# Optimization experiments

Measured on AMD Instinct MI355X. Metric: run time of the kernel, lower is better.

Reference implementation:

```python
import jax, jax.numpy as jnp
import numpy as np

B, N, DIM = 8, 8192, 256
HEADS, LOCAL_HEADS, WINDOW = 8, 1, 64
HD = DIM // HEADS  # 32
MLP_HIDDEN = 1024
EPS = 1e-5


def layer_norm(x, g, b):
    mu = jnp.mean(x, axis=-1, keepdims=True)
    var = jnp.var(x, axis=-1, keepdims=True)
    return (x - mu) * jax.lax.rsqrt(var + EPS) * g + b


def look_around(t, pad_value=0.0):
    # t: (b, nw, w, ...); concat windows [i-1, i, i+1] -> (b, nw, 3w, ...)
    nw = t.shape[1]
    pads = [(0, 0), (1, 1)] + [(0, 0)] * (t.ndim - 2)
    p = jnp.pad(t, pads, constant_values=pad_value)
    return jnp.concatenate([p[:, i:i + nw] for i in range(3)], axis=2)


def local_attn(q, k, v):
    # lucidrains LocalAttention, causal=False, look_backward=look_forward=1
    # q,k,v: (b_merged, n, d)
    b, n, d = q.shape
    nw = n // WINDOW
    scale = d ** -0.5
    bq = q.reshape(b, nw, WINDOW, d) * scale
    bk = look_around(k.reshape(b, nw, WINDOW, d))  # (b, nw, 3w, d)
    bv = look_around(v.reshape(b, nw, WINDOW, d))
    ticker = jnp.arange(n).reshape(1, nw, WINDOW)
    bq_k = look_around(ticker, pad_value=-1)       # (1, nw, 3w)
    pad_mask = (bq_k == -1)[:, :, None, :]         # (1, nw, 1, 3w)
    dots = jnp.einsum('bnie,bnje->bnij', bq, bk)   # (b, nw, w, 3w)
    dots = jnp.where(pad_mask, -1e9, dots)
    attn = jax.nn.softmax(dots, axis=-1)
    out = jnp.einsum('bnij,bnje->bnie', attn, bv)
    return out.reshape(b, n, d)


def linear_attn(q, k, v):
    # q,k,v: (b, h, n, d)
    d = q.shape[-1]
    qs = jax.nn.softmax(q, axis=-1) * d ** -0.5
    ks = jax.nn.softmax(k, axis=-2)
    ctx = jnp.einsum('bhnd,bhne->bhde', ks, v)     # (b, h, d, d) tiny
    return jnp.einsum('bhnd,bhde->bhne', qs, ctx)


def setup_inputs() -> dict:
    key = jax.random.key(0)
    ks = jax.random.split(key, 8)
    s = 0.02
    return {
        'x': jax.random.normal(ks[0], (B, N, DIM), jnp.float32),
        'norm1_g': jnp.ones((DIM,), jnp.float32),
        'norm1_b': jnp.zeros((DIM,), jnp.float32),
        'Wq': jax.random.normal(ks[1], (DIM, DIM), jnp.float32) * s,
        'Wkv': jax.random.normal(ks[2], (DIM, DIM), jnp.float32) * s,
        'Wproj': jax.random.normal(ks[3], (DIM, DIM), jnp.float32) * s,
        'bproj': jnp.zeros((DIM,), jnp.float32),
        'norm2_g': jnp.ones((DIM,), jnp.float32),
        'norm2_b': jnp.zeros((DIM,), jnp.float32),
        'W1': jax.random.normal(ks[4], (MLP_HIDDEN, DIM), jnp.float32) * s,
        'b1': jnp.zeros((MLP_HIDDEN,), jnp.float32),
        'W2': jax.random.normal(ks[5], (DIM, MLP_HIDDEN), jnp.float32) * s,
        'b2': jnp.zeros((DIM,), jnp.float32),
    }


def reference(x, norm1_g, norm1_b, Wq, Wkv, Wproj, bproj, norm2_g, norm2_b, W1, b1, W2, b2):
    b, n, c = x.shape
    h = layer_norm(x, norm1_g, norm1_b)
    q = h @ Wq.T
    kv = h @ Wkv.T  # k and v share the same projection in the original code
    split_heads = lambda t: t.reshape(b, n, HEADS, HD).transpose(0, 2, 1, 3)
    q, k, v = split_heads(q), split_heads(kv), split_heads(kv)
    lq, gq = q[:, :LOCAL_HEADS], q[:, LOCAL_HEADS:]
    lk, gk = k[:, :LOCAL_HEADS], k[:, LOCAL_HEADS:]
    lv, gv = v[:, :LOCAL_HEADS], v[:, LOCAL_HEADS:]
    lout = local_attn(lq.reshape(b * LOCAL_HEADS, n, HD),
                      lk.reshape(b * LOCAL_HEADS, n, HD),
                      lv.reshape(b * LOCAL_HEADS, n, HD)).reshape(b, LOCAL_HEADS, n, HD)
    gout = linear_attn(gq, gk, gv)
    attn = jnp.concatenate([lout, gout], axis=1)   # (b, H, n, hd)
    y = attn.transpose(0, 2, 1, 3).reshape(b, n, c) @ Wproj.T + bproj
    x = x + y
    h2 = layer_norm(x, norm2_g, norm2_b)
    m = jax.nn.gelu(h2 @ W1.T + b1, approximate=False) @ W2.T + b2
    return x + m
```

## Files before the change

### kernel.cpp

```cpp
#include <hip/hip_runtime.h>
#include <hip/hip_bf16.h>

typedef __bf16 bf16;
typedef __bf16 bf16x8 __attribute__((ext_vector_type(8)));
typedef float f32x4 __attribute__((ext_vector_type(4)));

__device__ __forceinline__ void gld16(const void* g, void* l) {
  __builtin_amdgcn_global_load_lds((const __attribute__((address_space(1))) void*)g,
                                   (__attribute__((address_space(3))) void*)l, 16, 0, 0);
}

__global__ void cvt_weights(const float* __restrict__ wq, const float* __restrict__ wkv,
                            const float* __restrict__ wp, const float* __restrict__ w1,
                            const float* __restrict__ w2,
                            bf16* __restrict__ wqkv, bf16* __restrict__ wpb,
                            bf16* __restrict__ w1b, bf16* __restrict__ w2b) {
  int i = blockIdx.x * 256 + threadIdx.x;
  if (i < 65536) wqkv[i] = (bf16)wq[i];
  else if (i < 131072) wqkv[i] = (bf16)wkv[i - 65536];
  else if (i < 196608) wpb[i - 131072] = (bf16)wp[i - 131072];
  else if (i < 458752) w1b[i - 196608] = (bf16)w1[i - 196608];
  else if (i < 720896) w2b[i - 458752] = (bf16)w2[i - 458752];
}

__launch_bounds__(256)
__global__ void ln_kernel(const float* __restrict__ x, const float* __restrict__ g,
                          const float* __restrict__ b, bf16* __restrict__ out) {
  const int row = blockIdx.x * 4 + (threadIdx.x >> 6);
  const int lane = threadIdx.x & 63;
  const float4 v = ((const float4*)(x + (long)row * 256))[lane];
  float s = v.x + v.y + v.z + v.w;
#pragma unroll
  for (int o = 1; o < 64; o <<= 1) s += __shfl_xor(s, o);
  const float mu = s * (1.f / 256.f);
  const float dx = v.x - mu, dy = v.y - mu, dz = v.z - mu, dw = v.w - mu;
  float q = dx * dx + dy * dy + dz * dz + dw * dw;
#pragma unroll
  for (int o = 1; o < 64; o <<= 1) q += __shfl_xor(q, o);
  const float rstd = rsqrtf(q * (1.f / 256.f) + 1e-5f);
  const float4 gg = ((const float4*)g)[lane];
  const float4 bb = ((const float4*)b)[lane];
  union { bf16 h[4]; uint2 u; } pk;
  pk.h[0] = (bf16)(dx * rstd * gg.x + bb.x);
  pk.h[1] = (bf16)(dy * rstd * gg.y + bb.y);
  pk.h[2] = (bf16)(dz * rstd * gg.z + bb.z);
  pk.h[3] = (bf16)(dw * rstd * gg.w + bb.w);
  *(uint2*)(out + (long)row * 256 + lane * 4) = pk.u;
}

template <int EPI, int MT, int NTILE, int KK, int NCHUNK>
__launch_bounds__(512, 4)
__global__ void gemm_bd(const bf16* __restrict__ A, const bf16* __restrict__ B,
                        void* C, const float* __restrict__ bias,
                        const float* res, int ldC) {
  constexpr int CW = NTILE / 8;
  constexpr int FM = MT / 16;
  constexpr int FN = CW / 16;
  constexpr int CK = KK / NCHUNK;
  constexpr int RSB = 2 * CK;
  constexpr int LROW = (RSB == 256) ? 8 : ((RSB == 512) ? 9 : 10);
  constexpr int CHB = MT * CK * 2;
  constexpr int ITER = CHB / (512 * 16);
  __shared__ bf16 lds[2 * MT * CK];
  const int tid = threadIdx.x;
  const int w = tid >> 6, lane = tid & 63;
  const int l15 = lane & 15, l4 = lane >> 4;
  const int swz = (l15 & 7) << 4;
  const long m0 = (long)blockIdx.x * MT;
  const int n_base = blockIdx.y * NTILE;
  const bf16* Bl = B + ((long)(n_base + w * CW + l15)) * KK + l4 * 8;

  f32x4 acc[FM][FN] = {};

  auto stage = [&](int c, int buf) {
#pragma unroll
    for (int it = 0; it < ITER; ++it) {
      const int p = it * 8192 + tid * 16;
      const int row = p >> LROW;
      const int colb = (p & (RSB - 1)) ^ ((row & 7) << 4);
      gld16((const char*)A + ((m0 + row) * KK + (long)c * CK) * 2 + colb,
            (char*)lds + buf * CHB + it * 8192 + w * 1024);
    }
  };

  stage(0, 0);
  asm volatile("s_waitcnt vmcnt(0)" ::: "memory");
  __syncthreads();

  for (int c = 0; c < NCHUNK; ++c) {
    if (c + 1 < NCHUNK) stage(c + 1, (c + 1) & 1);
    const char* base = (const char*)lds + (c & 1) * CHB;
#pragma unroll
    for (int kl = 0; kl < CK / 32; ++kl) {
      bf16x8 bfrag[FN];
#pragma unroll
      for (int fn = 0; fn < FN; ++fn)
        bfrag[fn] = *(const bf16x8*)(Bl + (long)fn * 16 * KK + c * CK + kl * 32);
      bf16x8 afrag[FM];
#pragma unroll
      for (int fm = 0; fm < FM; ++fm)
        afrag[fm] = *(const bf16x8*)(base + (fm * 16 + l15) * RSB + ((kl * 64 + l4 * 16) ^ swz));
#pragma unroll
      for (int fm = 0; fm < FM; ++fm)
#pragma unroll
        for (int fn = 0; fn < FN; ++fn)
          acc[fm][fn] = __builtin_amdgcn_mfma_f32_16x16x32_bf16(afrag[fm], bfrag[fn], acc[fm][fn], 0, 0, 0);
    }
    if (c + 1 < NCHUNK) {
      asm volatile("s_waitcnt vmcnt(0)" ::: "memory");
      __syncthreads();
    }
  }

#pragma unroll
  for (int fm = 0; fm < FM; ++fm)
#pragma unroll
    for (int fn = 0; fn < FN; ++fn)
#pragma unroll
      for (int r = 0; r < 4; ++r) {
        const long row = m0 + fm * 16 + l4 * 4 + r;
        const int col = n_base + w * CW + fn * 16 + l15;
        const long idx = row * ldC + col;
        const float v = acc[fm][fn][r];
        if constexpr (EPI == 0) {
          ((bf16*)C)[idx] = (bf16)v;
        } else if constexpr (EPI == 1) {
          ((float*)C)[idx] = v + bias[col] + res[idx];
        } else {
          const float t = v + bias[col];
          ((bf16*)C)[idx] = (bf16)(0.5f * t * (1.f + erff(t * 0.70710678118654752f)));
        }
      }
}

__launch_bounds__(256)
__global__ void lattn_kernel(const bf16* __restrict__ qkv, bf16* __restrict__ attn) {
  const int j = blockIdx.x, b = blockIdx.y;
  const int tid = threadIdx.x, w = tid >> 6, lane = tid & 63;
  __shared__ bf16 Qs[64 * 40];
  __shared__ bf16 Ks[192 * 40];
  __shared__ bf16 Kt[32 * 200];
  __shared__ bf16 Ps[4][16 * 200];
  const float scale = 0.17677669529663687f;
  const long base = (long)b * 8192 + (long)j * 64;
  for (int i = tid; i < 64 * 32; i += 256) {
    const int r = i >> 5, d = i & 31;
    Qs[r * 40 + d] = (bf16)((float)qkv[(base + r) * 512 + d] * scale);
  }
  for (int i = tid; i < 192 * 32; i += 256) {
    const int c = i >> 5, d = i & 31;
    const long tc = (long)j * 64 - 64 + c;
    float kv = 0.f;
    if (tc >= 0 && tc < 8192) kv = (float)qkv[((long)b * 8192 + tc) * 512 + 256 + d];
    const bf16 kb = (bf16)kv;
    Ks[c * 40 + d] = kb;
    Kt[d * 200 + c] = kb;
  }
  __syncthreads();
  const int l15 = lane & 15, l4 = lane >> 4;
  const bf16x8 aq = *(const bf16x8*)(Qs + (w * 16 + l15) * 40 + l4 * 8);
  const f32x4 zz = {0.f, 0.f, 0.f, 0.f};
  f32x4 S[12];
#pragma unroll
  for (int fn = 0; fn < 12; ++fn) {
    const bf16x8 bk = *(const bf16x8*)(Ks + (fn * 16 + l15) * 40 + l4 * 8);
    S[fn] = __builtin_amdgcn_mfma_f32_16x16x32_bf16(aq, bk, zz, 0, 0, 0);
  }
#pragma unroll
  for (int fn = 0; fn < 12; ++fn) {
    const long tc = (long)j * 64 - 64 + fn * 16 + l15;
    if (tc < 0 || tc >= 8192) { S[fn][0] = -1e9f; S[fn][1] = -1e9f; S[fn][2] = -1e9f; S[fn][3] = -1e9f; }
  }
  float sinv[4];
#pragma unroll
  for (int r = 0; r < 4; ++r) {
    float m = -1e30f;
#pragma unroll
    for (int fn = 0; fn < 12; ++fn) m = fmaxf(m, S[fn][r]);
#pragma unroll
    for (int o = 1; o < 16; o <<= 1) m = fmaxf(m, __shfl_xor(m, o));
    float s = 0.f;
#pragma unroll
    for (int fn = 0; fn < 12; ++fn) { const float e = __expf(S[fn][r] - m); S[fn][r] = e; s += e; }
#pragma unroll
    for (int o = 1; o < 16; o <<= 1) s += __shfl_xor(s, o);
    sinv[r] = 1.f / s;
  }
#pragma unroll
  for (int fn = 0; fn < 12; ++fn)
#pragma unroll
    for (int r = 0; r < 4; ++r)
      Ps[w][(l4 * 4 + r) * 200 + fn * 16 + l15] = (bf16)(S[fn][r] * sinv[r]);
  __syncthreads();
  f32x4 O[2] = {};
#pragma unroll
  for (int ks = 0; ks < 6; ++ks) {
    const bf16x8 ap = *(const bf16x8*)(Ps[w] + l15 * 200 + ks * 32 + l4 * 8);
#pragma unroll
    for (int fe = 0; fe < 2; ++fe) {
      const bf16x8 bv = *(const bf16x8*)(Kt + (fe * 16 + l15) * 200 + ks * 32 + l4 * 8);
      O[fe] = __builtin_amdgcn_mfma_f32_16x16x32_bf16(ap, bv, O[fe], 0, 0, 0);
    }
  }
#pragma unroll
  for (int fe = 0; fe < 2; ++fe)
#pragma unroll
    for (int r = 0; r < 4; ++r)
      attn[(base + w * 16 + l4 * 4 + r) * 256 + fe * 16 + l15] = (bf16)O[fe][r];
}

__launch_bounds__(256)
__global__ void ctx_kernel(const bf16* __restrict__ qkv, float* __restrict__ ctx,
                           float* __restrict__ S) {
  const int bh = blockIdx.x;
  const int b = bh / 7, h = bh % 7 + 1;
  const int tid = threadIdx.x;
  const int w = tid >> 6, lane = tid & 63;
  const int l15 = lane & 15, l4 = lane >> 4;
  __shared__ bf16 evT[32 * 264];
  __shared__ bf16 kT[48 * 264];
  __shared__ float red[4][32 * 48];
  const long n0 = (long)blockIdx.y * 256;
  const bf16* kp = qkv + ((long)b * 8192 + n0 + tid) * 512 + 256 + h * 32;
  bf16x8 kv[4];
#pragma unroll
  for (int c = 0; c < 4; ++c) kv[c] = *(const bf16x8*)(kp + c * 8);
#pragma unroll
  for (int i = 0; i < 16; ++i)
    kT[(32 + i) * 264 + tid] = (i == 0) ? (bf16)1.0f : (bf16)0.0f;
#pragma unroll
  for (int c = 0; c < 4; ++c)
#pragma unroll
    for (int j = 0; j < 8; ++j) {
      const int d = c * 8 + j;
      evT[d * 264 + tid] = (bf16)__expf((float)kv[c][j]);
      kT[d * 264 + tid] = kv[c][j];
    }
  __syncthreads();
  f32x4 acc[2][3] = {};
#pragma unroll
  for (int ks = 0; ks < 2; ++ks) {
    const int ncol = w * 64 + ks * 32 + l4 * 8;
    bf16x8 af[2], bb[3];
#pragma unroll
    for (int fm = 0; fm < 2; ++fm) af[fm] = *(const bf16x8*)(evT + (fm * 16 + l15) * 264 + ncol);
#pragma unroll
    for (int fe = 0; fe < 3; ++fe) bb[fe] = *(const bf16x8*)(kT + (fe * 16 + l15) * 264 + ncol);
#pragma unroll
    for (int fm = 0; fm < 2; ++fm)
#pragma unroll
      for (int fe = 0; fe < 3; ++fe)
        acc[fm][fe] = __builtin_amdgcn_mfma_f32_16x16x32_bf16(af[fm], bb[fe], acc[fm][fe], 0, 0, 0);
  }
#pragma unroll
  for (int fm = 0; fm < 2; ++fm)
#pragma unroll
    for (int fe = 0; fe < 3; ++fe)
#pragma unroll
      for (int r = 0; r < 4; ++r)
        red[w][(fm * 16 + l4 * 4 + r) * 48 + fe * 16 + l15] = acc[fm][fe][r];
  __syncthreads();
  for (int i = tid; i < 32 * 48; i += 256) {
    const float v = red[0][i] + red[1][i] + red[2][i] + red[3][i];
    const int d = i / 48, e = i - d * 48;
    if (e < 32) atomicAdd(ctx + (long)bh * 1024 + d * 32 + e, v);
    else if (e == 32) atomicAdd(S + bh * 32 + d, v);
  }
}

__launch_bounds__(256)
__global__ void lout_kernel(const bf16* __restrict__ qkv, const float* __restrict__ S,
                            const float* __restrict__ ctx, bf16* __restrict__ attn) {
  const int bh = blockIdx.x;
  const int b = bh / 7, h = bh % 7 + 1;
  const int tid = threadIdx.x;
  const int w = tid >> 6, lane = tid & 63;
  const int l15 = lane & 15, l4 = lane >> 4;
  __shared__ bf16 qs[256 * 40];
  __shared__ bf16 C2t[32 * 40];
  const long n0 = (long)blockIdx.y * 256;
  for (int i = tid; i < 1024; i += 256) {
    const int e = i >> 5, d = i & 31;
    C2t[e * 40 + d] = (bf16)(ctx[(long)bh * 1024 + d * 32 + e] / S[bh * 32 + d]);
  }
  const bf16* qp = qkv + ((long)b * 8192 + n0 + tid) * 512 + h * 32;
  bf16x8 qv[4];
#pragma unroll
  for (int c = 0; c < 4; ++c) qv[c] = *(const bf16x8*)(qp + c * 8);
  float qf[32];
#pragma unroll
  for (int c = 0; c < 4; ++c)
#pragma unroll
    for (int j = 0; j < 8; ++j) qf[c * 8 + j] = (float)qv[c][j];
  float m = qf[0];
#pragma unroll
  for (int d = 1; d < 32; ++d) m = fmaxf(m, qf[d]);
  float s = 0.f;
#pragma unroll
  for (int d = 0; d < 32; ++d) { qf[d] = __expf(qf[d] - m); s += qf[d]; }
  const float f = 0.17677669529663687f / s;
#pragma unroll
  for (int c = 0; c < 4; ++c) {
    bf16x8 o;
#pragma unroll
    for (int j = 0; j < 8; ++j) o[j] = (bf16)(qf[c * 8 + j] * f);
    *(bf16x8*)(qs + tid * 40 + c * 8) = o;
  }
  __syncthreads();
  f32x4 acc[4][2] = {};
  bf16x8 bfr[2];
#pragma unroll
  for (int fe = 0; fe < 2; ++fe) bfr[fe] = *(const bf16x8*)(C2t + (fe * 16 + l15) * 40 + l4 * 8);
#pragma unroll
  for (int fm = 0; fm < 4; ++fm) {
    const bf16x8 af = *(const bf16x8*)(qs + (w * 64 + fm * 16 + l15) * 40 + l4 * 8);
#pragma unroll
    for (int fe = 0; fe < 2; ++fe)
      acc[fm][fe] = __builtin_amdgcn_mfma_f32_16x16x32_bf16(af, bfr[fe], acc[fm][fe], 0, 0, 0);
  }
#pragma unroll
  for (int fm = 0; fm < 4; ++fm)
#pragma unroll
    for (int fe = 0; fe < 2; ++fe)
#pragma unroll
      for (int r = 0; r < 4; ++r)
        attn[((long)b * 8192 + n0 + w * 64 + fm * 16 + l4 * 4 + r) * 256 + h * 32 + fe * 16 + l15]
            = (bf16)acc[fm][fe][r];
}

extern "C" void kernel_launch(void* const* d_in, const int* in_sizes, int n_in,
                              void* d_out, int out_size, void* d_ws, size_t ws_size,
                              hipStream_t stream) {
  const float* x     = (const float*)d_in[0];
  const float* n1g   = (const float*)d_in[1];
  const float* n1b   = (const float*)d_in[2];
  const float* Wq    = (const float*)d_in[3];
  const float* Wkv   = (const float*)d_in[4];
  const float* Wproj = (const float*)d_in[5];
  const float* bproj = (const float*)d_in[6];
  const float* n2g   = (const float*)d_in[7];
  const float* n2b   = (const float*)d_in[8];
  const float* W1    = (const float*)d_in[9];
  const float* b1    = (const float*)d_in[10];
  const float* W2    = (const float*)d_in[11];
  const float* b2    = (const float*)d_in[12];
  float* out = (float*)d_out;
  char* ws = (char*)d_ws;

  bf16* wqkv   = (bf16*)(ws + 0);
  bf16* wprojb = (bf16*)(ws + 262144);
  bf16* w1b    = (bf16*)(ws + 393216);
  bf16* w2b    = (bf16*)(ws + 917504);
  float* Sbuf  = (float*)(ws + 1441792);
  float* ctx   = (float*)(ws + 1448960);
  bf16* hbuf   = (bf16*)(ws + 1685504);
  bf16* qkv    = (bf16*)(ws + 35239936);
  bf16* hidden = qkv;

  cvt_weights<<<2816, 256, 0, stream>>>(Wq, Wkv, Wproj, W1, W2, wqkv, wprojb, w1b, w2b);
  ln_kernel<<<16384, 256, 0, stream>>>(x, n1g, n1b, hbuf);
  gemm_bd<0, 64, 512, 256, 2><<<dim3(1024, 1), 512, 0, stream>>>(hbuf, wqkv, qkv, nullptr, nullptr, 512);
  hipMemsetAsync(Sbuf, 0, 7168 + 229376, stream);
  lattn_kernel<<<dim3(128, 8), 256, 0, stream>>>(qkv, hbuf);
  ctx_kernel<<<dim3(56, 32), 256, 0, stream>>>(qkv, ctx, Sbuf);
  lout_kernel<<<dim3(56, 32), 256, 0, stream>>>(qkv, Sbuf, ctx, hbuf);
  gemm_bd<1, 64, 256, 256, 2><<<dim3(1024, 1), 512, 0, stream>>>(hbuf, wprojb, out, bproj, x, 256);
  ln_kernel<<<16384, 256, 0, stream>>>(out, n2g, n2b, hbuf);
  gemm_bd<2, 64, 512, 256, 2><<<dim3(1024, 2), 512, 0, stream>>>(hbuf, w1b, hidden, b1, nullptr, 1024);
  gemm_bd<1, 64, 256, 1024, 4><<<dim3(1024, 1), 512, 0, stream>>>(hidden, w2b, out, b2, out, 256);
}
```

Before: 403.2 us.

## Make GEMMs persistent with register-resident weights and triple-buffered A pipeline

Replaces the one-tile-per-block GEMM with a persistent kernel. Each block loads its column slice of the bf16 weights into registers once, then streams many 64-row A tiles through a 3-stage LDS ring using async global-to-LDS loads. The epilogue stages results through LDS so global stores and residual/bias reads are 16-byte coalesced, and block IDs are remapped across XCDs. The cost is much higher register pressure from holding weights in registers, and fewer blocks launched, which reduces how much latency the hardware can hide.

```diff
diff --git a/kernel.cpp b/kernel.cpp
--- a/kernel.cpp
+++ b/kernel.cpp
@@ -48,89 +48,156 @@
   *(uint2*)(out + (long)row * 256 + lane * 4) = pk.u;
 }
 
-template <int EPI, int MT, int NTILE, int KK, int NCHUNK>
-__launch_bounds__(512, 4)
-__global__ void gemm_bd(const bf16* __restrict__ A, const bf16* __restrict__ B,
+template <int EPI, int NCG, int NCHUNK, int THREADS, int MSPLIT>
+__launch_bounds__(THREADS, (THREADS == 512) ? 4 : 2)
+__global__ void gemm_pb(const bf16* __restrict__ A, const bf16* __restrict__ Bw,
                         void* C, const float* __restrict__ bias,
                         const float* res, int ldC) {
-  constexpr int CW = NTILE / 8;
-  constexpr int FM = MT / 16;
-  constexpr int FN = CW / 16;
-  constexpr int CK = KK / NCHUNK;
-  constexpr int RSB = 2 * CK;
-  constexpr int LROW = (RSB == 256) ? 8 : ((RSB == 512) ? 9 : 10);
-  constexpr int CHB = MT * CK * 2;
-  constexpr int ITER = CHB / (512 * 16);
-  __shared__ bf16 lds[2 * MT * CK];
+  constexpr int WAVES = THREADS / 64;
+  constexpr int WR = (THREADS == 512) ? 2 : 1;
+  constexpr int WC = WAVES / WR;
+  constexpr int FN = (THREADS == 512) ? 2 : 1;
+  constexpr int FM = 64 / WR / 16;
+  constexpr int COLS = WC * FN * 16;
+  constexpr int KK = NCHUNK * 128;
+  constexpr int ITER = 64 * 128 * 2 / (THREADS * 16);
+  constexpr int TILES = 65536 / MSPLIT / 64;
+  constexpr int CHB = 64 * 128 * 2;
+  constexpr int BSZ = (EPI == 1) ? 64 * COLS * 4 : 64 * COLS * 2;
+  constexpr int NST = (EPI == 1) ? 12 : 2;
+  constexpr int NBLK = NCG * MSPLIT;
+  __shared__ char smem[3 * CHB + BSZ];
   const int tid = threadIdx.x;
   const int w = tid >> 6, lane = tid & 63;
   const int l15 = lane & 15, l4 = lane >> 4;
-  const int swz = (l15 & 7) << 4;
-  const long m0 = (long)blockIdx.x * MT;
-  const int n_base = blockIdx.y * NTILE;
-  const bf16* Bl = B + ((long)(n_base + w * CW + l15)) * KK + l4 * 8;
-
-  f32x4 acc[FM][FN] = {};
-
-  auto stage = [&](int c, int buf) {
+  const int wrow = w & (WR - 1), wcol = w / WR;
+  const int bid = blockIdx.x;
+  const int slot = (bid & 7) * (NBLK / 8) + (bid >> 3);
+  const int cg = slot % NCG;
+  const long strip0 = (long)(slot / NCG) * (65536 / MSPLIT);
+
+  const bf16* Bl = Bw + (long)(cg * COLS + wcol * FN * 16 + l15) * KK + l4 * 8;
+  bf16x8 Breg[NCHUNK][4][FN];
+#pragma unroll
+  for (int c = 0; c < NCHUNK; ++c)
+#pragma unroll
+    for (int kl = 0; kl < 4; ++kl)
+#pragma unroll
+      for (int fn = 0; fn < FN; ++fn)
+        Breg[c][kl][fn] = *(const bf16x8*)(Bl + (long)fn * 16 * KK + c * 128 + kl * 32);
+
+  float bias_r[FN];
+  if constexpr (EPI == 2) {
+#pragma unroll
+    for (int fn = 0; fn < FN; ++fn)
+      bias_r[fn] = bias[cg * COLS + wcol * FN * 16 + fn * 16 + l15];
+  }
+
+  auto stage = [&](int m, int c, int buf) {
 #pragma unroll
     for (int it = 0; it < ITER; ++it) {
-      const int p = it * 8192 + tid * 16;
-      const int row = p >> LROW;
-      const int colb = (p & (RSB - 1)) ^ ((row & 7) << 4);
-      gld16((const char*)A + ((m0 + row) * KK + (long)c * CK) * 2 + colb,
-            (char*)lds + buf * CHB + it * 8192 + w * 1024);
+      const int p = it * (THREADS * 16) + tid * 16;
+      const int row = p >> 8;
+      const int colb = (p & 255) ^ ((row & 7) << 4);
+      gld16((const char*)A + ((strip0 + m * 64 + row) * KK + c * 128) * 2 + colb,
+            smem + buf * CHB + it * (THREADS * 16) + w * 1024);
     }
   };
 
-  stage(0, 0);
-  asm volatile("s_waitcnt vmcnt(0)" ::: "memory");
-  __syncthreads();
-
-  for (int c = 0; c < NCHUNK; ++c) {
-    if (c + 1 < NCHUNK) stage(c + 1, (c + 1) & 1);
-    const char* base = (const char*)lds + (c & 1) * CHB;
-#pragma unroll
-    for (int kl = 0; kl < CK / 32; ++kl) {
-      bf16x8 bfrag[FN];
-#pragma unroll
-      for (int fn = 0; fn < FN; ++fn)
-        bfrag[fn] = *(const bf16x8*)(Bl + (long)fn * 16 * KK + c * CK + kl * 32);
-      bf16x8 afrag[FM];
-#pragma unroll
-      for (int fm = 0; fm < FM; ++fm)
-        afrag[fm] = *(const bf16x8*)(base + (fm * 16 + l15) * RSB + ((kl * 64 + l4 * 16) ^ swz));
-#pragma unroll
-      for (int fm = 0; fm < FM; ++fm)
-#pragma unroll
-        for (int fn = 0; fn < FN; ++fn)
-          acc[fm][fn] = __builtin_amdgcn_mfma_f32_16x16x32_bf16(afrag[fm], bfrag[fn], acc[fm][fn], 0, 0, 0);
+  f32x4 acc[FM][FN] = {};
+  stage(0, 0, 0);
+  stage(0, 1, 1);
+
+  for (int m = 0; m < TILES; ++m) {
+#pragma unroll
+    for (int c = 0; c < NCHUNK; ++c) {
+      const int s = m * NCHUNK + c;
+      if (m == 0 || c >= 2) {
+        asm volatile("s_waitcnt vmcnt(%0)" ::"i"(ITER) : "memory");
+      } else {
+        asm volatile("s_waitcnt vmcnt(%0)" ::"i"(ITER + NST) : "memory");
+      }
+      __syncthreads();
+      {
+        int c2 = c + 2, m2 = m;
+        if (c2 >= NCHUNK) { c2 -= NCHUNK; ++m2; }
+        if (m2 < TILES) stage(m2, c2, (s + 2) % 3);
+      }
+      const char* Ab = smem + (s % 3) * CHB;
+#pragma unroll
+      for (int kl = 0; kl < 4; ++kl) {
+        bf16x8 af[FM];
+#pragma unroll
+        for (int fm = 0; fm < FM; ++fm) {
+          const int arow = wrow * (64 / WR) + fm * 16 + l15;
+          af[fm] = *(const bf16x8*)(Ab + arow * 256 + ((kl * 64 + l4 * 16) ^ ((l15 & 7) << 4)));
+        }
+#pragma unroll
+        for (int fm = 0; fm < FM; ++fm)
+#pragma unroll
+          for (int fn = 0; fn < FN; ++fn)
+            acc[fm][fn] = __builtin_amdgcn_mfma_f32_16x16x32_bf16(af[fm], Breg[c][kl][fn],
+                                                                  acc[fm][fn], 0, 0, 0);
+      }
+      if (c == NCHUNK - 1) {
+        if constexpr (EPI == 1) {
+          float* fb = (float*)(smem + 3 * CHB);
+#pragma unroll
+          for (int fm = 0; fm < FM; ++fm)
+#pragma unroll
+            for (int fn = 0; fn < FN; ++fn)
+#pragma unroll
+              for (int r = 0; r < 4; ++r)
+                fb[(wrow * (64 / WR) + fm * 16 + l4 * 4 + r) * COLS +
+                   wcol * FN * 16 + fn * 16 + l15] = acc[fm][fn][r];
+          __syncthreads();
+#pragma unroll
+          for (int it = 0; it < 64 * COLS * 4 / (THREADS * 16); ++it) {
+            const int off = it * (THREADS * 16) + tid * 16;
+            const int row = off / (COLS * 4);
+            const int colb = off % (COLS * 4);
+            const long gb = ((strip0 + m * 64 + row) * ldC + cg * COLS) * 4 + colb;
+            float4 v = *(const float4*)(smem + 3 * CHB + off);
+            const float4 rr = *(const float4*)((const char*)res + gb);
+            const float4 bv = *(const float4*)((const char*)bias + cg * COLS * 4 + colb);
+            v.x += rr.x + bv.x; v.y += rr.y + bv.y;
+            v.z += rr.z + bv.z; v.w += rr.w + bv.w;
+            *(float4*)((char*)C + gb) = v;
+          }
+        } else {
+          bf16* bb = (bf16*)(smem + 3 * CHB);
+#pragma unroll
+          for (int fm = 0; fm < FM; ++fm)
+#pragma unroll
+            for (int fn = 0; fn < FN; ++fn)
+#pragma unroll
+              for (int r = 0; r < 4; ++r) {
+                float v = acc[fm][fn][r];
+                if constexpr (EPI == 2) {
+                  v += bias_r[fn];
+                  v = 0.5f * v * (1.f + erff(v * 0.70710678118654752f));
+                }
+                bb[(wrow * (64 / WR) + fm * 16 + l4 * 4 + r) * COLS +
+                   wcol * FN * 16 + fn * 16 + l15] = (bf16)v;
+              }
+          __syncthreads();
+#pragma unroll
+          for (int it = 0; it < 64 * COLS * 2 / (THREADS * 16); ++it) {
+            const int off = it * (THREADS * 16) + tid * 16;
+            const int row = off / (COLS * 2);
+            const int colb = off % (COLS * 2);
+            *(uint4*)((char*)C + ((strip0 + m * 64 + row) * ldC + cg * COLS) * 2 + colb) =
+                *(const uint4*)(smem + 3 * CHB + off);
+          }
+        }
+#pragma unroll
+        for (int fm = 0; fm < FM; ++fm)
+#pragma unroll
+          for (int fn = 0; fn < FN; ++fn)
+            acc[fm][fn] = f32x4{0.f, 0.f, 0.f, 0.f};
+      }
     }
-    if (c + 1 < NCHUNK) {
-      asm volatile("s_waitcnt vmcnt(0)" ::: "memory");
-      __syncthreads();
-    }
-  }
-
-#pragma unroll
-  for (int fm = 0; fm < FM; ++fm)
-#pragma unroll
-    for (int fn = 0; fn < FN; ++fn)
-#pragma unroll
-      for (int r = 0; r < 4; ++r) {
-        const long row = m0 + fm * 16 + l4 * 4 + r;
-        const int col = n_base + w * CW + fn * 16 + l15;
-        const long idx = row * ldC + col;
-        const float v = acc[fm][fn][r];
-        if constexpr (EPI == 0) {
-          ((bf16*)C)[idx] = (bf16)v;
-        } else if constexpr (EPI == 1) {
-          ((float*)C)[idx] = v + bias[col] + res[idx];
-        } else {
-          const float t = v + bias[col];
-          ((bf16*)C)[idx] = (bf16)(0.5f * t * (1.f + erff(t * 0.70710678118654752f)));
-        }
-      }
+  }
 }
 
 __launch_bounds__(256)
@@ -359,13 +426,13 @@
 
   cvt_weights<<<2816, 256, 0, stream>>>(Wq, Wkv, Wproj, W1, W2, wqkv, wprojb, w1b, w2b);
   ln_kernel<<<16384, 256, 0, stream>>>(x, n1g, n1b, hbuf);
-  gemm_bd<0, 64, 512, 256, 2><<<dim3(1024, 1), 512, 0, stream>>>(hbuf, wqkv, qkv, nullptr, nullptr, 512);
+  gemm_pb<0, 4, 2, 512, 128><<<512, 512, 0, stream>>>(hbuf, wqkv, qkv, nullptr, nullptr, 512);
   hipMemsetAsync(Sbuf, 0, 7168 + 229376, stream);
   lattn_kernel<<<dim3(128, 8), 256, 0, stream>>>(qkv, hbuf);
   ctx_kernel<<<dim3(56, 32), 256, 0, stream>>>(qkv, ctx, Sbuf);
   lout_kernel<<<dim3(56, 32), 256, 0, stream>>>(qkv, Sbuf, ctx, hbuf);
-  gemm_bd<1, 64, 256, 256, 2><<<dim3(1024, 1), 512, 0, stream>>>(hbuf, wprojb, out, bproj, x, 256);
+  gemm_pb<1, 2, 2, 512, 256><<<512, 512, 0, stream>>>(hbuf, wprojb, out, bproj, x, 256);
   ln_kernel<<<16384, 256, 0, stream>>>(out, n2g, n2b, hbuf);
-  gemm_bd<2, 64, 512, 256, 2><<<dim3(1024, 2), 512, 0, stream>>>(hbuf, w1b, hidden, b1, nullptr, 1024);
-  gemm_bd<1, 64, 256, 1024, 4><<<dim3(1024, 1), 512, 0, stream>>>(hidden, w2b, out, b2, out, 256);
-}
+  gemm_pb<2, 8, 2, 512, 64><<<512, 512, 0, stream>>>(hbuf, w1b, hidden, b1, nullptr, 1024);
+  gemm_pb<1, 4, 8, 256, 256><<<1024, 256, 0, stream>>>(hidden, w2b, out, b2, out, 256);
+}
```

Result: faster. 332.4 us (-17.6%).
